# Kernel tuning notes

Measured on AMD Instinct MI355X. Metric: run time of the kernel, lower is better.

Reference implementation:

```python
import jax, jax.numpy as jnp
import numpy as np

N, E, D_IN, H, D = 170000, 1200000, 128, 4, 32
NEG_SLOPE = 0.2


def setup_inputs() -> dict:
    key = jax.random.key(0)
    ks = jax.random.split(key, 8)
    x = jax.random.normal(ks[0], (N, D_IN), dtype=jnp.float32)
    # xavier-normal-ish scale for linear weights
    W_embed = jax.random.normal(ks[1], (D_IN, H * D), dtype=jnp.float32) * (2.0 / (D_IN + H * D)) ** 0.5
    a_src = jax.random.normal(ks[2], (H, D), dtype=jnp.float32) * (2.0 / (1 + H * D)) ** 0.5
    a_dst = jax.random.normal(ks[3], (H, D), dtype=jnp.float32) * (2.0 / (1 + H * D)) ** 0.5
    W_lin = jax.random.normal(ks[4], (D_IN, H * D), dtype=jnp.float32) * (2.0 / (D_IN + H * D)) ** 0.5
    bias = jnp.zeros((H * D,), dtype=jnp.float32)
    src = jax.random.randint(ks[5], (E,), 0, N, dtype=jnp.int32)
    dst = jax.random.randint(ks[6], (E,), 0, N, dtype=jnp.int32)
    return {"x": x, "W_embed": W_embed, "a_src": a_src, "a_dst": a_dst,
            "W_lin": W_lin, "bias": bias, "src": src, "dst": dst}


def reference(x, W_embed, a_src, a_dst, W_lin, bias, src, dst):
    n = x.shape[0]
    # node projections: [N, H, D]
    h = (x @ W_embed).reshape(n, H, D)
    dot_src = jnp.einsum('nhd,hd->nh', h, a_src)  # [N, H]
    dot_dst = jnp.einsum('nhd,hd->nh', h, a_dst)  # [N, H]
    # edge attention logits: leaky_relu(dot_src[u] + dot_dst[v])  [E, H]
    z = dot_src[src] + dot_dst[dst]
    logit = jnp.where(z >= 0, z, NEG_SLOPE * z)
    # edge softmax over incoming edges of each destination node
    m = jax.ops.segment_max(logit, dst, num_segments=n)          # [N, H]
    e = jnp.exp(logit - m[dst])                                   # [E, H]
    denom = jax.ops.segment_sum(e, dst, num_segments=n)          # [N, H]
    prob = e / denom[dst]                                         # [E, H]
    # weighted scatter-sum aggregation: sum_e prob_e * h[src_e]
    msg = h[src] * prob[:, :, None]                               # [E, H, D]
    out = jax.ops.segment_sum(msg, dst, num_segments=n)          # [N, H, D]
    out = out.reshape(n, H * D)
    out = out + x @ W_lin
    out = out + bias[None, :]
    return out
```

## Files before the change

kernel.cpp:

```cpp
#include <hip/hip_runtime.h>
#include <hip/hip_bf16.h>

static constexpr int   N_NODES   = 170000;
static constexpr int   E_EDGES   = 1200000;
static constexpr float NEG_SLOPE = 0.2f;

typedef __attribute__((ext_vector_type(8))) short bfrag8;
typedef __attribute__((ext_vector_type(4))) float facc4;

__device__ __forceinline__ short f2bf(float f) {
    __hip_bfloat16 h = __float2bfloat16(f);
    return *reinterpret_cast<short*>(&h);
}

__global__ void wt_convert_kernel(const float* __restrict__ We,
                                  const float* __restrict__ Wl,
                                  short* __restrict__ WtG)
{
    const int k = blockIdx.x;
    const int t = threadIdx.x;
    if (t < 128) WtG[t * 128 + k] = f2bf(We[k * 128 + t]);
    else         WtG[t * 128 + k] = f2bf(Wl[k * 128 + (t - 128)]);
}

__global__ void init_kernel(int* __restrict__ deg) {
    int i = blockIdx.x * blockDim.x + threadIdx.x;
    if (i < N_NODES) deg[i] = 0;
}

__global__ void hist_kernel(const int* __restrict__ dst, int* __restrict__ deg) {
    int e = blockIdx.x * blockDim.x + threadIdx.x;
    if (e < E_EDGES) atomicAdd(&deg[dst[e]], 1);
}

__global__ __launch_bounds__(256) void scan_local_kernel(
    const int* __restrict__ deg, int* __restrict__ row_ptr, int* __restrict__ bsum)
{
    __shared__ int sh[256];
    const int t = threadIdx.x;
    const int base = blockIdx.x * 1024 + t * 4;
    int v0 = (base + 0 < N_NODES) ? deg[base + 0] : 0;
    int v1 = (base + 1 < N_NODES) ? deg[base + 1] : 0;
    int v2 = (base + 2 < N_NODES) ? deg[base + 2] : 0;
    int v3 = (base + 3 < N_NODES) ? deg[base + 3] : 0;
    const int tot = v0 + v1 + v2 + v3;
    sh[t] = tot;
    __syncthreads();
    for (int off = 1; off < 256; off <<= 1) {
        int add = (t >= off) ? sh[t - off] : 0;
        __syncthreads();
        sh[t] += add;
        __syncthreads();
    }
    const int excl = sh[t] - tot;
    if (base + 0 < N_NODES) row_ptr[base + 0] = excl;
    if (base + 1 < N_NODES) row_ptr[base + 1] = excl + v0;
    if (base + 2 < N_NODES) row_ptr[base + 2] = excl + v0 + v1;
    if (base + 3 < N_NODES) row_ptr[base + 3] = excl + v0 + v1 + v2;
    if (t == 255) bsum[blockIdx.x] = sh[255];
}

__global__ __launch_bounds__(256) void scan_block_kernel(
    const int* __restrict__ bsum, int* __restrict__ boff, int nblk)
{
    __shared__ int sh[256];
    const int t = threadIdx.x;
    const int v = (t < nblk) ? bsum[t] : 0;
    sh[t] = v;
    __syncthreads();
    for (int off = 1; off < 256; off <<= 1) {
        int add = (t >= off) ? sh[t - off] : 0;
        __syncthreads();
        sh[t] += add;
        __syncthreads();
    }
    boff[t] = sh[t] - v;
}

__global__ void scan_add_kernel(int* __restrict__ row_ptr,
                                const int* __restrict__ boff,
                                int* __restrict__ fill)
{
    int i = blockIdx.x * blockDim.x + threadIdx.x;
    if (i < N_NODES) {
        int v = row_ptr[i] + boff[i >> 10];
        row_ptr[i] = v;
        fill[i] = v;
    }
    if (i == 0) row_ptr[N_NODES] = E_EDGES;
}

static constexpr int LDA = 136;

__global__ __launch_bounds__(256) void mfma_gemm_kernel(
    const float* __restrict__ x,
    const short* __restrict__ WtG,
    const float* __restrict__ bias,
    const float* __restrict__ a_srcp,
    const float* __restrict__ a_dstp,
    short* __restrict__ hbuf,
    float* __restrict__ dsrc,
    float* __restrict__ ddst,
    float* __restrict__ outp)
{
    __shared__ short As[64 * LDA];
    __shared__ short Bs[128 * LDA];
    const int tid  = threadIdx.x;
    const int half = blockIdx.y;
    const long row0 = (long)blockIdx.x * 64;

    #pragma unroll
    for (int it = 0; it < 8; ++it) {
        const int idx = it * 256 + tid;
        const int n   = idx >> 4;
        const int kc  = (idx & 15) * 8;
        *(int4*)&Bs[n * LDA + kc] =
            *(const int4*)&WtG[(half * 128 + n) * 128 + kc];
    }
    #pragma unroll
    for (int it = 0; it < 8; ++it) {
        const int idx = it * 256 + tid;
        const int r = idx >> 5;
        const int j = idx & 31;
        const long row = row0 + r;
        float4 v = make_float4(0.f, 0.f, 0.f, 0.f);
        if (row < N_NODES) v = ((const float4*)x)[row * 32 + j];
        uint u0 = (uint)(unsigned short)f2bf(v.x) | ((uint)(unsigned short)f2bf(v.y) << 16);
        uint u1 = (uint)(unsigned short)f2bf(v.z) | ((uint)(unsigned short)f2bf(v.w) << 16);
        *(uint2*)&As[r * LDA + j * 4] = make_uint2(u0, u1);
    }
    __syncthreads();

    const int w    = tid >> 6;
    const int l    = tid & 63;
    const int col  = l & 15;
    const int quad = l >> 4;
    const int mrow = w * 16 + col;

    facc4 acc[8];
    #pragma unroll
    for (int t = 0; t < 8; ++t) acc[t] = (facc4)(0.f);

    #pragma unroll
    for (int ks = 0; ks < 4; ++ks) {
        const bfrag8 a = *(const bfrag8*)&As[mrow * LDA + ks * 32 + quad * 8];
        #pragma unroll
        for (int t = 0; t < 8; ++t) {
            const bfrag8 b = *(const bfrag8*)&Bs[(t * 16 + col) * LDA + ks * 32 + quad * 8];
            acc[t] = __builtin_amdgcn_mfma_f32_16x16x32_bf16(a, b, acc[t], 0, 0, 0);
        }
    }

    const long rbase = row0 + w * 16 + quad * 4;
    if (half == 0) {
        float as[8], ad[8];
        #pragma unroll
        for (int t = 0; t < 8; ++t) {
            as[t] = a_srcp[t * 16 + col];
            ad[t] = a_dstp[t * 16 + col];
        }
        #pragma unroll
        for (int r = 0; r < 4; ++r) {
            const long m = rbase + r;
            if (m >= N_NODES) continue;
            float ps[4] = {0.f, 0.f, 0.f, 0.f};
            float pd[4] = {0.f, 0.f, 0.f, 0.f};
            #pragma unroll
            for (int t = 0; t < 8; ++t) {
                hbuf[m * 128 + t * 16 + col] = f2bf(acc[t][r]);
                ps[t >> 1] += acc[t][r] * as[t];
                pd[t >> 1] += acc[t][r] * ad[t];
            }
            #pragma unroll
            for (int mask = 1; mask < 16; mask <<= 1) {
                #pragma unroll
                for (int hh = 0; hh < 4; ++hh) {
                    ps[hh] += __shfl_xor(ps[hh], mask, 16);
                    pd[hh] += __shfl_xor(pd[hh], mask, 16);
                }
            }
            if (col == 0) {
                ((float4*)dsrc)[m] = make_float4(ps[0], ps[1], ps[2], ps[3]);
                ((float4*)ddst)[m] = make_float4(pd[0], pd[1], pd[2], pd[3]);
            }
        }
    } else {
        #pragma unroll
        for (int t = 0; t < 8; ++t) {
            const float bv = bias[t * 16 + col];
            #pragma unroll
            for (int r = 0; r < 4; ++r) {
                const long m = rbase + r;
                if (m < N_NODES) outp[m * 128 + t * 16 + col] = acc[t][r] + bv;
            }
        }
    }
}

__global__ void csr_place_kernel(const int* __restrict__ src,
                                 const int* __restrict__ dst,
                                 int* __restrict__ fill,
                                 int* __restrict__ srcs)
{
    int e = blockIdx.x * blockDim.x + threadIdx.x;
    if (e >= E_EDGES) return;
    const int p = atomicAdd(&fill[dst[e]], 1);
    srcs[p] = src[e];
}

__global__ __launch_bounds__(256) void agg_kernel(
    const int* __restrict__ row_ptr, const int* __restrict__ srcs,
    const float* __restrict__ dsrc, const float* __restrict__ ddst,
    const short* __restrict__ hbuf, float* __restrict__ outp)
{
    const long node = (long)blockIdx.x * 4 + (threadIdx.x >> 6);
    if (node >= N_NODES) return;
    const int lane = threadIdx.x & 63;
    const int head = lane >> 4;
    const int start = __builtin_amdgcn_readfirstlane(row_ptr[node]);
    const int end   = __builtin_amdgcn_readfirstlane(row_ptr[node + 1]);
    if (start == end) return;

    const float dd = ddst[node * 4 + head];

    float a0 = 0.f, a1 = 0.f, dn = 0.f;
    for (int j = start; j < end; ++j) {
        const int s = __builtin_amdgcn_readfirstlane(srcs[j]);
        float z = dsrc[s * 4 + head] + dd;
        z = (z >= 0.f) ? z : NEG_SLOPE * z;
        const float wgt = __expf(z);
        dn += wgt;
        const uint hv = *(const uint*)&hbuf[(long)s * 128 + (lane << 1)];
        a0 += wgt * __uint_as_float(hv << 16);
        a1 += wgt * __uint_as_float(hv & 0xFFFF0000u);
    }
    const float inv = 1.f / dn;
    float2* op = (float2*)&outp[node * 128 + (lane << 1)];
    float2 o = *op;
    o.x += a0 * inv;
    o.y += a1 * inv;
    *op = o;
}

extern "C" void kernel_launch(void* const* d_in, const int* in_sizes, int n_in,
                              void* d_out, int out_size, void* d_ws, size_t ws_size,
                              hipStream_t stream)
{
    const float* x       = (const float*)d_in[0];
    const float* W_embed = (const float*)d_in[1];
    const float* a_src   = (const float*)d_in[2];
    const float* a_dst   = (const float*)d_in[3];
    const float* W_lin   = (const float*)d_in[4];
    const float* bias    = (const float*)d_in[5];
    const int*   src     = (const int*)d_in[6];
    const int*   dst     = (const int*)d_in[7];
    float* outp = (float*)d_out;

    char* ws = (char*)d_ws;
    short* WtG   = (short*)ws;  ws += (size_t)256 * 128 * sizeof(short);
    short* hbuf  = (short*)ws;  ws += (size_t)N_NODES * 128 * sizeof(short);
    int*   srcs  = (int*)ws;    ws += (size_t)E_EDGES * sizeof(int);
    float* dsrc  = (float*)ws;  ws += (size_t)N_NODES * 4 * sizeof(float);
    float* ddst  = (float*)ws;  ws += (size_t)N_NODES * 4 * sizeof(float);
    int*   deg   = (int*)ws;    ws += (size_t)N_NODES * sizeof(int);
    int*   fill  = (int*)ws;    ws += (size_t)N_NODES * sizeof(int);
    int*   rowp  = (int*)ws;    ws += (size_t)(N_NODES + 16) * sizeof(int);
    int*   bsum  = (int*)ws;    ws += 256 * sizeof(int);
    int*   boff  = (int*)ws;    ws += 256 * sizeof(int);

    const int SCAN_BLKS = (N_NODES + 1023) / 1024;

    wt_convert_kernel<<<128, 256, 0, stream>>>(W_embed, W_lin, WtG);
    init_kernel<<<(N_NODES + 255) / 256, 256, 0, stream>>>(deg);
    hist_kernel<<<(E_EDGES + 255) / 256, 256, 0, stream>>>(dst, deg);
    scan_local_kernel<<<SCAN_BLKS, 256, 0, stream>>>(deg, rowp, bsum);
    scan_block_kernel<<<1, 256, 0, stream>>>(bsum, boff, SCAN_BLKS);
    scan_add_kernel<<<(N_NODES + 255) / 256, 256, 0, stream>>>(rowp, boff, fill);

    dim3 ggrid((N_NODES + 63) / 64, 2);
    mfma_gemm_kernel<<<ggrid, 256, 0, stream>>>(
        x, WtG, bias, a_src, a_dst, hbuf, dsrc, ddst, outp);

    csr_place_kernel<<<(E_EDGES + 255) / 256, 256, 0, stream>>>(src, dst, fill, srcs);

    agg_kernel<<<(N_NODES + 3) / 4, 256, 0, stream>>>(
        rowp, srcs, dsrc, ddst, hbuf, outp);
}
```

Measured before the change: 459.9 us.

## Fuse weight convert with degree init, share x tile across GEMM halves, batch aggregation loads

The weight conversion and degree-zeroing kernels are merged into one launch. The GEMM now runs both output halves in one block, so each x tile is loaded and converted to bf16 once instead of twice, at the cost of a serial loop over the halves with extra barriers. The aggregation kernel loads up to 64 source indices per wave with one coalesced read and broadcasts them with readlane. It issues gathers for 8 edges before accumulating to hide memory latency, and masks the padded edges to zero weight.

```diff
diff --git a/kernel.cpp b/kernel.cpp
--- a/kernel.cpp
+++ b/kernel.cpp
@@ -13,18 +13,18 @@
     return *reinterpret_cast<short*>(&h);
 }
 
-__global__ void wt_convert_kernel(const float* __restrict__ We,
-                                  const float* __restrict__ Wl,
-                                  short* __restrict__ WtG)
-{
-    const int k = blockIdx.x;
+__global__ void wt_init_kernel(const float* __restrict__ We,
+                               const float* __restrict__ Wl,
+                               short* __restrict__ WtG,
+                               int* __restrict__ deg)
+{
     const int t = threadIdx.x;
-    if (t < 128) WtG[t * 128 + k] = f2bf(We[k * 128 + t]);
-    else         WtG[t * 128 + k] = f2bf(Wl[k * 128 + (t - 128)]);
-}
-
-__global__ void init_kernel(int* __restrict__ deg) {
-    int i = blockIdx.x * blockDim.x + threadIdx.x;
+    if (blockIdx.x < 128) {
+        const int k = blockIdx.x;
+        if (t < 128) WtG[t * 128 + k] = f2bf(We[k * 128 + t]);
+        else         WtG[t * 128 + k] = f2bf(Wl[k * 128 + (t - 128)]);
+    }
+    const int i = blockIdx.x * 256 + t;
     if (i < N_NODES) deg[i] = 0;
 }
 
@@ -106,17 +106,8 @@
     __shared__ short As[64 * LDA];
     __shared__ short Bs[128 * LDA];
     const int tid  = threadIdx.x;
-    const int half = blockIdx.y;
     const long row0 = (long)blockIdx.x * 64;
 
-    #pragma unroll
-    for (int it = 0; it < 8; ++it) {
-        const int idx = it * 256 + tid;
-        const int n   = idx >> 4;
-        const int kc  = (idx & 15) * 8;
-        *(int4*)&Bs[n * LDA + kc] =
-            *(const int4*)&WtG[(half * 128 + n) * 128 + kc];
-    }
     #pragma unroll
     for (int it = 0; it < 8; ++it) {
         const int idx = it * 256 + tid;
@@ -129,7 +120,6 @@
         uint u1 = (uint)(unsigned short)f2bf(v.z) | ((uint)(unsigned short)f2bf(v.w) << 16);
         *(uint2*)&As[r * LDA + j * 4] = make_uint2(u0, u1);
     }
-    __syncthreads();
 
     const int w    = tid >> 6;
     const int l    = tid & 63;
@@ -137,61 +127,75 @@
     const int quad = l >> 4;
     const int mrow = w * 16 + col;
 
-    facc4 acc[8];
     #pragma unroll
-    for (int t = 0; t < 8; ++t) acc[t] = (facc4)(0.f);
-
-    #pragma unroll
-    for (int ks = 0; ks < 4; ++ks) {
-        const bfrag8 a = *(const bfrag8*)&As[mrow * LDA + ks * 32 + quad * 8];
+    for (int half = 0; half < 2; ++half) {
         #pragma unroll
-        for (int t = 0; t < 8; ++t) {
-            const bfrag8 b = *(const bfrag8*)&Bs[(t * 16 + col) * LDA + ks * 32 + quad * 8];
-            acc[t] = __builtin_amdgcn_mfma_f32_16x16x32_bf16(a, b, acc[t], 0, 0, 0);
+        for (int it = 0; it < 8; ++it) {
+            const int idx = it * 256 + tid;
+            const int n   = idx >> 4;
+            const int kc  = (idx & 15) * 8;
+            *(int4*)&Bs[n * LDA + kc] =
+                *(const int4*)&WtG[(half * 128 + n) * 128 + kc];
         }
-    }
-
-    const long rbase = row0 + w * 16 + quad * 4;
-    if (half == 0) {
-        float as[8], ad[8];
+        __syncthreads();
+
+        facc4 acc[8];
         #pragma unroll
-        for (int t = 0; t < 8; ++t) {
-            as[t] = a_srcp[t * 16 + col];
-            ad[t] = a_dstp[t * 16 + col];
-        }
+        for (int t = 0; t < 8; ++t) acc[t] = (facc4)(0.f);
+
         #pragma unroll
-        for (int r = 0; r < 4; ++r) {
-            const long m = rbase + r;
-            if (m >= N_NODES) continue;
-            float ps[4] = {0.f, 0.f, 0.f, 0.f};
-            float pd[4] = {0.f, 0.f, 0.f, 0.f};
+        for (int ks = 0; ks < 4; ++ks) {
+            const bfrag8 a = *(const bfrag8*)&As[mrow * LDA + ks * 32 + quad * 8];
             #pragma unroll
             for (int t = 0; t < 8; ++t) {
-                hbuf[m * 128 + t * 16 + col] = f2bf(acc[t][r]);
-                ps[t >> 1] += acc[t][r] * as[t];
-                pd[t >> 1] += acc[t][r] * ad[t];
-            }
-            #pragma unroll
-            for (int mask = 1; mask < 16; mask <<= 1) {
-                #pragma unroll
-                for (int hh = 0; hh < 4; ++hh) {
-                    ps[hh] += __shfl_xor(ps[hh], mask, 16);
-                    pd[hh] += __shfl_xor(pd[hh], mask, 16);
-                }
-            }
-            if (col == 0) {
-                ((float4*)dsrc)[m] = make_float4(ps[0], ps[1], ps[2], ps[3]);
-                ((float4*)ddst)[m] = make_float4(pd[0], pd[1], pd[2], pd[3]);
+                const bfrag8 b = *(const bfrag8*)&Bs[(t * 16 + col) * LDA + ks * 32 + quad * 8];
+                acc[t] = __builtin_amdgcn_mfma_f32_16x16x32_bf16(a, b, acc[t], 0, 0, 0);
             }
         }
-    } else {
-        #pragma unroll
-        for (int t = 0; t < 8; ++t) {
-            const float bv = bias[t * 16 + col];
+
+        const long rbase = row0 + w * 16 + quad * 4;
+        if (half == 0) {
+            float as[8], ad[8];
+            #pragma unroll
+            for (int t = 0; t < 8; ++t) {
+                as[t] = a_srcp[t * 16 + col];
+                ad[t] = a_dstp[t * 16 + col];
+            }
             #pragma unroll
             for (int r = 0; r < 4; ++r) {
                 const long m = rbase + r;
-                if (m < N_NODES) outp[m * 128 + t * 16 + col] = acc[t][r] + bv;
+                if (m >= N_NODES) continue;
+                float ps[4] = {0.f, 0.f, 0.f, 0.f};
+                float pd[4] = {0.f, 0.f, 0.f, 0.f};
+                #pragma unroll
+                for (int t = 0; t < 8; ++t) {
+                    hbuf[m * 128 + t * 16 + col] = f2bf(acc[t][r]);
+                    ps[t >> 1] += acc[t][r] * as[t];
+                    pd[t >> 1] += acc[t][r] * ad[t];
+                }
+                #pragma unroll
+                for (int mask = 1; mask < 16; mask <<= 1) {
+                    #pragma unroll
+                    for (int hh = 0; hh < 4; ++hh) {
+                        ps[hh] += __shfl_xor(ps[hh], mask, 16);
+                        pd[hh] += __shfl_xor(pd[hh], mask, 16);
+                    }
+                }
+                if (col == 0) {
+                    ((float4*)dsrc)[m] = make_float4(ps[0], ps[1], ps[2], ps[3]);
+                    ((float4*)ddst)[m] = make_float4(pd[0], pd[1], pd[2], pd[3]);
+                }
+            }
+            __syncthreads();
+        } else {
+            #pragma unroll
+            for (int t = 0; t < 8; ++t) {
+                const float bv = bias[t * 16 + col];
+                #pragma unroll
+                for (int r = 0; r < 4; ++r) {
+                    const long m = rbase + r;
+                    if (m < N_NODES) outp[m * 128 + t * 16 + col] = acc[t][r] + bv;
+                }
             }
         }
     }
@@ -217,6 +221,7 @@
     if (node >= N_NODES) return;
     const int lane = threadIdx.x & 63;
     const int head = lane >> 4;
+    const int c2   = lane << 1;
     const int start = __builtin_amdgcn_readfirstlane(row_ptr[node]);
     const int end   = __builtin_amdgcn_readfirstlane(row_ptr[node + 1]);
     if (start == end) return;
@@ -224,18 +229,41 @@
     const float dd = ddst[node * 4 + head];
 
     float a0 = 0.f, a1 = 0.f, dn = 0.f;
-    for (int j = start; j < end; ++j) {
-        const int s = __builtin_amdgcn_readfirstlane(srcs[j]);
-        float z = dsrc[s * 4 + head] + dd;
-        z = (z >= 0.f) ? z : NEG_SLOPE * z;
-        const float wgt = __expf(z);
-        dn += wgt;
-        const uint hv = *(const uint*)&hbuf[(long)s * 128 + (lane << 1)];
-        a0 += wgt * __uint_as_float(hv << 16);
-        a1 += wgt * __uint_as_float(hv & 0xFFFF0000u);
-    }
+
+#define EDGE_LOAD(i) \
+    const int   s##i = __builtin_amdgcn_readlane(sv, k + i); \
+    const float e##i = dsrc[s##i * 4 + head]; \
+    const uint  h##i = *(const uint*)&hbuf[(long)s##i * 128 + c2];
+
+#define EDGE_ACC(i) { \
+    float z = e##i + dd; \
+    z = (z >= 0.f) ? z : NEG_SLOPE * z; \
+    float wv = __expf(z); \
+    if (k + i >= chunk) wv = 0.f; \
+    dn += wv; \
+    a0 = fmaf(wv, __uint_as_float(h##i << 16),        a0); \
+    a1 = fmaf(wv, __uint_as_float(h##i & 0xFFFF0000u), a1); }
+
+    int j = start;
+    while (j < end) {
+        const int rem   = end - j;
+        const int chunk = rem < 64 ? rem : 64;
+        int idx = j + lane;
+        if (idx > end - 1) idx = end - 1;
+        const int sv = srcs[idx];
+        for (int k = 0; k < chunk; k += 8) {
+            EDGE_LOAD(0) EDGE_LOAD(1) EDGE_LOAD(2) EDGE_LOAD(3)
+            EDGE_LOAD(4) EDGE_LOAD(5) EDGE_LOAD(6) EDGE_LOAD(7)
+            EDGE_ACC(0) EDGE_ACC(1) EDGE_ACC(2) EDGE_ACC(3)
+            EDGE_ACC(4) EDGE_ACC(5) EDGE_ACC(6) EDGE_ACC(7)
+        }
+        j += chunk;
+    }
+#undef EDGE_LOAD
+#undef EDGE_ACC
+
     const float inv = 1.f / dn;
-    float2* op = (float2*)&outp[node * 128 + (lane << 1)];
+    float2* op = (float2*)&outp[node * 128 + c2];
     float2 o = *op;
     o.x += a0 * inv;
     o.y += a1 * inv;
@@ -270,15 +298,13 @@
 
     const int SCAN_BLKS = (N_NODES + 1023) / 1024;
 
-    wt_convert_kernel<<<128, 256, 0, stream>>>(W_embed, W_lin, WtG);
-    init_kernel<<<(N_NODES + 255) / 256, 256, 0, stream>>>(deg);
+    wt_init_kernel<<<(N_NODES + 255) / 256, 256, 0, stream>>>(W_embed, W_lin, WtG, deg);
     hist_kernel<<<(E_EDGES + 255) / 256, 256, 0, stream>>>(dst, deg);
     scan_local_kernel<<<SCAN_BLKS, 256, 0, stream>>>(deg, rowp, bsum);
     scan_block_kernel<<<1, 256, 0, stream>>>(bsum, boff, SCAN_BLKS);
     scan_add_kernel<<<(N_NODES + 255) / 256, 256, 0, stream>>>(rowp, boff, fill);
 
-    dim3 ggrid((N_NODES + 63) / 64, 2);
-    mfma_gemm_kernel<<<ggrid, 256, 0, stream>>>(
+    mfma_gemm_kernel<<<(N_NODES + 63) / 64, 256, 0, stream>>>(
         x, WtG, bias, a_src, a_dst, hbuf, dsrc, ddst, outp);
 
     csr_place_kernel<<<(E_EDGES + 255) / 256, 256, 0, stream>>>(src, dst, fill, srcs);
```

Measured after the change: 429.9 us. -6.5%, faster.
